# Kernel optimization log

Hardware: AMD Instinct MI355X
Metric: run time of the kernel (lower is better)

## Reference

```python
import jax, jax.numpy as jnp
import numpy as np

DIM = 3            # point feature dim (xyz)
POS_HID = 64       # pos_mlp hidden
ATTN_HID = DIM * 4 # attn_mlp hidden (mult=4)
N_NBR = 16         # points per group
GROUPS = 512       # groups per batch element
MLP_D = N_NBR * DIM  # 48


def setup_inputs() -> dict:
    key = jax.random.key(0)
    ks = jax.random.split(key, 20)
    B = 32
    s = lambda *sh: 1.0 / np.sqrt(sh[0])
    inp = {
        "original_points": jax.random.normal(ks[0], (B, GROUPS, DIM), jnp.float32),
        "data": jax.random.normal(ks[1], (B, GROUPS, N_NBR, DIM), jnp.float32),
        # PointTransformerLayer params
        "w_qkv": jax.random.normal(ks[2], (DIM, DIM * 3), jnp.float32) * s(DIM),
        "pos_w1": jax.random.normal(ks[3], (3, POS_HID), jnp.float32) * s(3),
        "pos_b1": jnp.zeros((POS_HID,), jnp.float32),
        "pos_w2": jax.random.normal(ks[4], (POS_HID, DIM), jnp.float32) * s(POS_HID),
        "pos_b2": jnp.zeros((DIM,), jnp.float32),
        "attn_w1": jax.random.normal(ks[5], (DIM, ATTN_HID), jnp.float32) * s(DIM),
        "attn_b1": jnp.zeros((ATTN_HID,), jnp.float32),
        "attn_w2": jax.random.normal(ks[6], (ATTN_HID, DIM), jnp.float32) * s(ATTN_HID),
        "attn_b2": jnp.zeros((DIM,), jnp.float32),
        # downstream MLP params
        "mlp_w1": jax.random.normal(ks[7], (MLP_D, MLP_D), jnp.float32) * s(MLP_D),
        "mlp_b1": jnp.zeros((MLP_D,), jnp.float32),
        "mlp_w2": jax.random.normal(ks[8], (MLP_D, MLP_D), jnp.float32) * s(MLP_D),
        "mlp_b2": jnp.zeros((MLP_D,), jnp.float32),
        "mlp_w3": jax.random.normal(ks[9], (MLP_D, 1), jnp.float32) * s(MLP_D),
        "mlp_b3": jnp.zeros((1,), jnp.float32),
    }
    return inp


def reference(original_points, data, w_qkv, pos_w1, pos_b1, pos_w2, pos_b2,
              attn_w1, attn_b1, attn_w2, attn_b2,
              mlp_w1, mlp_b1, mlp_w2, mlp_b2, mlp_w3, mlp_b3):
    B, G, n, d = data.shape
    x = data.reshape(B * G, n, d)          # (BG, n, 3)
    pos = x[:, :, :3]                       # pos == features here (f=3)

    # Point-transformer vector attention
    qkv = x @ w_qkv                          # (BG, n, 9)
    q, k, v = jnp.split(qkv, 3, axis=-1)
    rel_pos = pos[:, :, None, :] - pos[:, None, :, :]              # (BG, n, n, 3)
    rel_emb = jax.nn.relu(rel_pos @ pos_w1 + pos_b1) @ pos_w2 + pos_b2  # (BG, n, n, 3)
    qk_rel = q[:, :, None, :] - k[:, None, :, :]                   # (BG, n, n, 3)
    v_ij = v[:, None, :, :] + rel_emb                              # (BG, n, n, 3)
    sim = jax.nn.relu((qk_rel + rel_emb) @ attn_w1 + attn_b1) @ attn_w2 + attn_b2
    attn = jax.nn.softmax(sim, axis=-2)                            # softmax over j
    agg = jnp.einsum('bijd,bijd->bid', attn, v_ij)                 # (BG, n, 3)

    # regroup into (B, 512, 48) exactly as stack(split(512, dim=0))
    sa = agg.reshape(B, G, n * d)
    h = jax.nn.relu(sa @ mlp_w1 + mlp_b1)
    h = jax.nn.relu(h @ mlp_w2 + mlp_b2)
    return h @ mlp_w3 + mlp_b3              # (B, 512, 1)
```

## Files before the change

kernel.cpp:

```cpp
#include <hip/hip_runtime.h>


#define ASTRIDE 68

__global__ __launch_bounds__(256) void pt_main(
    const float* __restrict__ data,
    const float* __restrict__ wqkv,
    const float* __restrict__ pw1,
    const float* __restrict__ pb1,
    const float* __restrict__ pw2,
    const float* __restrict__ pb2,
    const float* __restrict__ aw1,
    const float* __restrict__ ab1,
    const float* __restrict__ aw2,
    const float* __restrict__ ab2,
    const float* __restrict__ mw1,
    const float* __restrict__ mb1,
    const float* __restrict__ mw2,
    const float* __restrict__ mb2,
    const float* __restrict__ mw3,
    const float* __restrict__ mb3,
    float* __restrict__ out)
{
    __shared__ float s_pos[48];
    __shared__ float s_q[48], s_k[48], s_v[48];
    __shared__ float s_sa[48], s_h1[48];
    __shared__ float a1[16 * ASTRIDE];
    __shared__ float a2[16 * ASTRIDE];

    const int g = blockIdx.x;
    const int t = threadIdx.x;

    if (t < 48) s_pos[t] = data[g * 48 + t];
    __syncthreads();

    if (t < 48) {
        const int sec = t >> 4, p = t & 15;
        const float x0 = s_pos[p*3+0], x1 = s_pos[p*3+1], x2 = s_pos[p*3+2];
        float* dst = (sec == 0) ? s_q : (sec == 1) ? s_k : s_v;
        #pragma unroll
        for (int c = 0; c < 3; ++c) {
            dst[p*3+c] = fmaf(x0, wqkv[0*9 + sec*3 + c],
                         fmaf(x1, wqkv[1*9 + sec*3 + c],
                         x2 * wqkv[2*9 + sec*3 + c]));
        }
    }

    {
        const int i  = t >> 4;
        const int hc = (t & 15) << 2;
        const float x0 = s_pos[i*3+0], x1 = s_pos[i*3+1], x2 = s_pos[i*3+2];
        float4 va, vb;
        #pragma unroll
        for (int c = 0; c < 4; ++c) {
            const int h = hc + c;
            const float s = fmaf(x0, pw1[h], fmaf(x1, pw1[64+h], x2 * pw1[128+h]));
            (&vb.x)[c] = s;
            (&va.x)[c] = s + pb1[h];
        }
        *(float4*)&a1[i * ASTRIDE + hc] = va;
        *(float4*)&a2[i * ASTRIDE + hc] = vb;
    }
    __syncthreads();

    const int i = t >> 4, j = t & 15;

    float e0 = pb2[0], e1 = pb2[1], e2 = pb2[2];
    #pragma unroll
    for (int c16 = 0; c16 < 16; ++c16) {
        const int h0 = c16 * 4;
        const float4 ai = *(const float4*)&a1[i * ASTRIDE + h0];
        const float4 aj = *(const float4*)&a2[j * ASTRIDE + h0];
        #pragma unroll
        for (int c = 0; c < 4; ++c) {
            const float hh = fmaxf((&ai.x)[c] - (&aj.x)[c], 0.0f);
            e0 = fmaf(hh, pw2[(h0+c)*3+0], e0);
            e1 = fmaf(hh, pw2[(h0+c)*3+1], e1);
            e2 = fmaf(hh, pw2[(h0+c)*3+2], e2);
        }
    }

    const float vi0 = s_v[j*3+0] + e0, vi1 = s_v[j*3+1] + e1, vi2 = s_v[j*3+2] + e2;
    const float si0 = s_q[i*3+0] - s_k[j*3+0] + e0;
    const float si1 = s_q[i*3+1] - s_k[j*3+1] + e1;
    const float si2 = s_q[i*3+2] - s_k[j*3+2] + e2;

    float m0 = ab2[0], m1 = ab2[1], m2 = ab2[2];
    #pragma unroll
    for (int gg = 0; gg < 12; ++gg) {
        float hg = fmaf(si0, aw1[gg], fmaf(si1, aw1[12+gg], fmaf(si2, aw1[24+gg], ab1[gg])));
        hg = fmaxf(hg, 0.0f);
        m0 = fmaf(hg, aw2[gg*3+0], m0);
        m1 = fmaf(hg, aw2[gg*3+1], m1);
        m2 = fmaf(hg, aw2[gg*3+2], m2);
    }

    float x0 = m0, x1 = m1, x2 = m2;
    #pragma unroll
    for (int mk = 1; mk < 16; mk <<= 1) {
        x0 = fmaxf(x0, __shfl_xor(x0, mk));
        x1 = fmaxf(x1, __shfl_xor(x1, mk));
        x2 = fmaxf(x2, __shfl_xor(x2, mk));
    }
    float p0 = __expf(m0 - x0), p1 = __expf(m1 - x1), p2 = __expf(m2 - x2);

    float n0 = p0 * vi0, n1 = p1 * vi1, n2 = p2 * vi2;
    float d0 = p0, d1 = p1, d2 = p2;
    #pragma unroll
    for (int mk = 1; mk < 16; mk <<= 1) {
        n0 += __shfl_xor(n0, mk);  d0 += __shfl_xor(d0, mk);
        n1 += __shfl_xor(n1, mk);  d1 += __shfl_xor(d1, mk);
        n2 += __shfl_xor(n2, mk);  d2 += __shfl_xor(d2, mk);
    }
    if (j == 0) {
        s_sa[i*3+0] = n0 / d0;
        s_sa[i*3+1] = n1 / d1;
        s_sa[i*3+2] = n2 / d2;
    }
    __syncthreads();

    if (t < 48) {
        float h1 = mb1[t];
        #pragma unroll
        for (int c = 0; c < 48; ++c) h1 = fmaf(s_sa[c], mw1[c*48+t], h1);
        s_h1[t] = fmaxf(h1, 0.0f);
    }
    __syncthreads();

    float fv = 0.0f;
    if (t < 48) {
        float h2 = mb2[t];
        #pragma unroll
        for (int c = 0; c < 48; ++c) h2 = fmaf(s_h1[c], mw2[c*48+t], h2);
        h2 = fmaxf(h2, 0.0f);
        fv = h2 * mw3[t];
    }
    if (t < 64) {
        #pragma unroll
        for (int mk = 1; mk < 64; mk <<= 1) fv += __shfl_xor(fv, mk);
        if (t == 0) out[g] = fv + mb3[0];
    }
}

extern "C" void kernel_launch(void* const* d_in, const int* in_sizes, int n_in,
                              void* d_out, int out_size, void* d_ws, size_t ws_size,
                              hipStream_t stream) {
    const float* data = (const float*)d_in[1];
    const int groups = out_size;

    pt_main<<<groups, 256, 0, stream>>>(
        data,
        (const float*)d_in[2],  (const float*)d_in[3],  (const float*)d_in[4],
        (const float*)d_in[5],  (const float*)d_in[6],  (const float*)d_in[7],
        (const float*)d_in[8],  (const float*)d_in[9],  (const float*)d_in[10],
        (const float*)d_in[11], (const float*)d_in[12], (const float*)d_in[13],
        (const float*)d_in[14], (const float*)d_in[15], (const float*)d_in[16],
        (float*)d_out);
}
```

Baseline: 156.6 us.

## Compute pos-MLP second layer and attn first layer via bf16 MFMA

Folds pos_w2 and attn_w1 into one combined 64x16 weight matrix in bf16. The relu hidden activations for all i,j pairs are multiplied by it with MFMA 16x16x32, giving the rel_emb and attn-hidden contributions together. The q and k terms of the attention first layer are precomputed per point, and biases are folded. The softmax drops max subtraction, uses raw exp2/rcp, and replaces shuffle reductions with DPP row reductions. This trades bf16 precision and overflow safety (no max subtraction) for removing most per-thread scalar FMAs.

```diff
diff --git a/kernel.cpp b/kernel.cpp
--- a/kernel.cpp
+++ b/kernel.cpp
@@ -2,6 +2,38 @@
 
 
 #define ASTRIDE 68
+#define ESTRIDE 264
+#define BSTRIDE 72
+
+typedef float f32x4v __attribute__((ext_vector_type(4)));
+typedef short s16x8  __attribute__((ext_vector_type(8)));
+
+union AFrag { int i[4]; s16x8 s; };
+
+__device__ __forceinline__ unsigned short f2bf_rne(float f) {
+    unsigned u = __builtin_bit_cast(unsigned, f);
+    u += 0x7fffu + ((u >> 16) & 1u);
+    return (unsigned short)(u >> 16);
+}
+
+__device__ __forceinline__ int pack_bf2(float lo, float hi) {
+    return __builtin_amdgcn_perm(__builtin_bit_cast(int, hi),
+                                 __builtin_bit_cast(int, lo), 0x07060302);
+}
+
+__device__ __forceinline__ float dpp_add16(float x) {
+    float s = x;
+    int t;
+    t = __builtin_amdgcn_update_dpp(0, __builtin_bit_cast(int, s), 0x121, 0xf, 0xf, false);
+    s += __builtin_bit_cast(float, t);
+    t = __builtin_amdgcn_update_dpp(0, __builtin_bit_cast(int, s), 0x122, 0xf, 0xf, false);
+    s += __builtin_bit_cast(float, t);
+    t = __builtin_amdgcn_update_dpp(0, __builtin_bit_cast(int, s), 0x124, 0xf, 0xf, false);
+    s += __builtin_bit_cast(float, t);
+    t = __builtin_amdgcn_update_dpp(0, __builtin_bit_cast(int, s), 0x128, 0xf, 0xf, false);
+    s += __builtin_bit_cast(float, t);
+    return s;
+}
 
 __global__ __launch_bounds__(256) void pt_main(
     const float* __restrict__ data,
@@ -22,14 +54,20 @@
     const float* __restrict__ mb3,
     float* __restrict__ out)
 {
-    __shared__ float s_pos[48];
-    __shared__ float s_q[48], s_k[48], s_v[48];
-    __shared__ float s_sa[48], s_h1[48];
-    __shared__ float a1[16 * ASTRIDE];
-    __shared__ float a2[16 * ASTRIDE];
-
-    const int g = blockIdx.x;
-    const int t = threadIdx.x;
+    __shared__ __attribute__((aligned(16))) float s_pos[48];
+    __shared__ __attribute__((aligned(16))) float s_q[48], s_k[48], s_v[48];
+    __shared__ __attribute__((aligned(16))) float s_qa[16*12], s_ka[16*12];
+    __shared__ __attribute__((aligned(16))) float s_sa[48], s_h1[48];
+    __shared__ __attribute__((aligned(16))) float a1[16*ASTRIDE], a2[16*ASTRIDE];
+    __shared__ __attribute__((aligned(16))) unsigned short s_Bc[16*BSTRIDE];
+    __shared__ __attribute__((aligned(16))) float s_e[16*ESTRIDE];
+
+    const int g    = blockIdx.x;
+    const int t    = threadIdx.x;
+    const int lane = t & 63;
+    const int wv   = t >> 6;
+    const int quad = lane >> 4;
+    const int ln   = lane & 15;
 
     if (t < 48) s_pos[t] = data[g * 48 + t];
     __syncthreads();
@@ -40,16 +78,18 @@
         float* dst = (sec == 0) ? s_q : (sec == 1) ? s_k : s_v;
         #pragma unroll
         for (int c = 0; c < 3; ++c) {
-            dst[p*3+c] = fmaf(x0, wqkv[0*9 + sec*3 + c],
-                         fmaf(x1, wqkv[1*9 + sec*3 + c],
-                         x2 * wqkv[2*9 + sec*3 + c]));
+            float v = fmaf(x0, wqkv[0*9 + sec*3 + c],
+                      fmaf(x1, wqkv[1*9 + sec*3 + c],
+                      x2 * wqkv[2*9 + sec*3 + c]));
+            if (sec == 2) v += pb2[c];
+            dst[p*3+c] = v;
         }
     }
 
     {
-        const int i  = t >> 4;
+        const int ii = t >> 4;
         const int hc = (t & 15) << 2;
-        const float x0 = s_pos[i*3+0], x1 = s_pos[i*3+1], x2 = s_pos[i*3+2];
+        const float x0 = s_pos[ii*3+0], x1 = s_pos[ii*3+1], x2 = s_pos[ii*3+2];
         float4 va, vb;
         #pragma unroll
         for (int c = 0; c < 4; ++c) {
@@ -58,64 +98,117 @@
             (&vb.x)[c] = s;
             (&va.x)[c] = s + pb1[h];
         }
-        *(float4*)&a1[i * ASTRIDE + hc] = va;
-        *(float4*)&a2[i * ASTRIDE + hc] = vb;
+        *(float4*)&a1[ii * ASTRIDE + hc] = va;
+        *(float4*)&a2[ii * ASTRIDE + hc] = vb;
+    }
+
+    {
+        const int k  = t & 63;
+        const int n0 = (t >> 6) << 2;
+        const float w0 = pw2[k*3+0], w1 = pw2[k*3+1], w2v = pw2[k*3+2];
+        #pragma unroll
+        for (int d = 0; d < 4; ++d) {
+            const int n = n0 + d;
+            float val;
+            if (n < 3)       val = (n == 0) ? w0 : (n == 1) ? w1 : w2v;
+            else if (n < 15) { const int a = n - 3;
+                               val = fmaf(w0, aw1[a], fmaf(w1, aw1[12+a], w2v * aw1[24+a])); }
+            else             val = 0.0f;
+            s_Bc[n * BSTRIDE + k] = f2bf_rne(val);
+        }
+    }
+    __syncthreads();
+
+    if (t < 32) {
+        const int p = t & 15;
+        const float* src = (t < 16) ? s_q : s_k;
+        const float x0 = src[p*3+0], x1 = src[p*3+1], x2 = src[p*3+2];
+        float* dst = (t < 16) ? s_qa : s_ka;
+        #pragma unroll
+        for (int gg = 0; gg < 12; ++gg) {
+            float v = fmaf(x0, aw1[gg], fmaf(x1, aw1[12+gg], x2 * aw1[24+gg]));
+            if (t < 16)
+                v += fmaf(pb2[0], aw1[gg], fmaf(pb2[1], aw1[12+gg], pb2[2]*aw1[24+gg])) + ab1[gg];
+            dst[p*12+gg] = v;
+        }
+    }
+
+    s16x8 bfrag0 = *(const s16x8*)&s_Bc[ln * BSTRIDE + quad * 8];
+    s16x8 bfrag1 = *(const s16x8*)&s_Bc[ln * BSTRIDE + 32 + quad * 8];
+
+    #pragma unroll
+    for (int tau = 0; tau < 4; ++tau) {
+        const int it = (wv << 2) + tau;
+        f32x4v acc = {0.f, 0.f, 0.f, 0.f};
+        #pragma unroll
+        for (int kc = 0; kc < 2; ++kc) {
+            const int off = kc * 32 + quad * 8;
+            const float4 u0 = *(const float4*)&a1[it * ASTRIDE + off];
+            const float4 u1 = *(const float4*)&a1[it * ASTRIDE + off + 4];
+            const float4 w0 = *(const float4*)&a2[ln * ASTRIDE + off];
+            const float4 w1 = *(const float4*)&a2[ln * ASTRIDE + off + 4];
+            const float r0 = fmaxf(u0.x - w0.x, 0.f);
+            const float r1 = fmaxf(u0.y - w0.y, 0.f);
+            const float r2 = fmaxf(u0.z - w0.z, 0.f);
+            const float r3 = fmaxf(u0.w - w0.w, 0.f);
+            const float r4 = fmaxf(u1.x - w1.x, 0.f);
+            const float r5 = fmaxf(u1.y - w1.y, 0.f);
+            const float r6 = fmaxf(u1.z - w1.z, 0.f);
+            const float r7 = fmaxf(u1.w - w1.w, 0.f);
+            AFrag af;
+            af.i[0] = pack_bf2(r0, r1);
+            af.i[1] = pack_bf2(r2, r3);
+            af.i[2] = pack_bf2(r4, r5);
+            af.i[3] = pack_bf2(r6, r7);
+            acc = __builtin_amdgcn_mfma_f32_16x16x32_bf16(
+                      af.s, (kc == 0) ? bfrag0 : bfrag1, acc, 0, 0, 0);
+        }
+        *(f32x4v*)&s_e[ln * ESTRIDE + (wv << 6) + (tau << 4) + (quad << 2)] = acc;
     }
     __syncthreads();
 
     const int i = t >> 4, j = t & 15;
 
-    float e0 = pb2[0], e1 = pb2[1], e2 = pb2[2];
-    #pragma unroll
-    for (int c16 = 0; c16 < 16; ++c16) {
-        const int h0 = c16 * 4;
-        const float4 ai = *(const float4*)&a1[i * ASTRIDE + h0];
-        const float4 aj = *(const float4*)&a2[j * ASTRIDE + h0];
-        #pragma unroll
-        for (int c = 0; c < 4; ++c) {
-            const float hh = fmaxf((&ai.x)[c] - (&aj.x)[c], 0.0f);
-            e0 = fmaf(hh, pw2[(h0+c)*3+0], e0);
-            e1 = fmaf(hh, pw2[(h0+c)*3+1], e1);
-            e2 = fmaf(hh, pw2[(h0+c)*3+2], e2);
-        }
-    }
-
-    const float vi0 = s_v[j*3+0] + e0, vi1 = s_v[j*3+1] + e1, vi2 = s_v[j*3+2] + e2;
-    const float si0 = s_q[i*3+0] - s_k[j*3+0] + e0;
-    const float si1 = s_q[i*3+1] - s_k[j*3+1] + e1;
-    const float si2 = s_q[i*3+2] - s_k[j*3+2] + e2;
+    union F12 { float4 v[3]; float f[12]; } qa_, ka_;
+    qa_.v[0] = *(const float4*)&s_qa[i*12 + 0];
+    qa_.v[1] = *(const float4*)&s_qa[i*12 + 4];
+    qa_.v[2] = *(const float4*)&s_qa[i*12 + 8];
+    ka_.v[0] = *(const float4*)&s_ka[j*12 + 0];
+    ka_.v[1] = *(const float4*)&s_ka[j*12 + 4];
+    ka_.v[2] = *(const float4*)&s_ka[j*12 + 8];
+
+    const float e0 = s_e[0*ESTRIDE + t];
+    const float e1 = s_e[1*ESTRIDE + t];
+    const float e2 = s_e[2*ESTRIDE + t];
+    const float vi0 = s_v[j*3+0] + e0;
+    const float vi1 = s_v[j*3+1] + e1;
+    const float vi2 = s_v[j*3+2] + e2;
 
     float m0 = ab2[0], m1 = ab2[1], m2 = ab2[2];
     #pragma unroll
     for (int gg = 0; gg < 12; ++gg) {
-        float hg = fmaf(si0, aw1[gg], fmaf(si1, aw1[12+gg], fmaf(si2, aw1[24+gg], ab1[gg])));
-        hg = fmaxf(hg, 0.0f);
+        const float hg = fmaxf(qa_.f[gg] - ka_.f[gg] + s_e[(3+gg)*ESTRIDE + t], 0.f);
         m0 = fmaf(hg, aw2[gg*3+0], m0);
         m1 = fmaf(hg, aw2[gg*3+1], m1);
         m2 = fmaf(hg, aw2[gg*3+2], m2);
     }
 
-    float x0 = m0, x1 = m1, x2 = m2;
-    #pragma unroll
-    for (int mk = 1; mk < 16; mk <<= 1) {
-        x0 = fmaxf(x0, __shfl_xor(x0, mk));
-        x1 = fmaxf(x1, __shfl_xor(x1, mk));
-        x2 = fmaxf(x2, __shfl_xor(x2, mk));
-    }
-    float p0 = __expf(m0 - x0), p1 = __expf(m1 - x1), p2 = __expf(m2 - x2);
-
-    float n0 = p0 * vi0, n1 = p1 * vi1, n2 = p2 * vi2;
-    float d0 = p0, d1 = p1, d2 = p2;
-    #pragma unroll
-    for (int mk = 1; mk < 16; mk <<= 1) {
-        n0 += __shfl_xor(n0, mk);  d0 += __shfl_xor(d0, mk);
-        n1 += __shfl_xor(n1, mk);  d1 += __shfl_xor(d1, mk);
-        n2 += __shfl_xor(n2, mk);  d2 += __shfl_xor(d2, mk);
-    }
+    const float L2E = 1.44269504f;
+    const float p0 = __builtin_amdgcn_exp2f(m0 * L2E);
+    const float p1 = __builtin_amdgcn_exp2f(m1 * L2E);
+    const float p2 = __builtin_amdgcn_exp2f(m2 * L2E);
+
+    const float n0 = dpp_add16(p0 * vi0);
+    const float n1 = dpp_add16(p1 * vi1);
+    const float n2 = dpp_add16(p2 * vi2);
+    const float d0 = dpp_add16(p0);
+    const float d1 = dpp_add16(p1);
+    const float d2 = dpp_add16(p2);
+
     if (j == 0) {
-        s_sa[i*3+0] = n0 / d0;
-        s_sa[i*3+1] = n1 / d1;
-        s_sa[i*3+2] = n2 / d2;
+        s_sa[i*3+0] = n0 * __builtin_amdgcn_rcpf(d0);
+        s_sa[i*3+1] = n1 * __builtin_amdgcn_rcpf(d1);
+        s_sa[i*3+2] = n2 * __builtin_amdgcn_rcpf(d2);
     }
     __syncthreads();
 
```

New measurement: 188.5 us. +20.3%, slower.
